# Kernel tuning notes

Hardware: AMD Instinct MI355X
Metric: run time of the kernel (lower is better)

Reference implementation:

```python
import jax, jax.numpy as jnp
import numpy as np

K = 1024
D = 256
BETA = 0.25


def setup_inputs() -> dict:
    key = jax.random.key(0)
    k1, k2 = jax.random.split(key)
    inputs = jax.random.normal(k1, (16, D, 4096), dtype=jnp.float32)  # (B, D, T)
    # embedding.weight.data.uniform_(-1/K, 1/K)
    weight = jax.random.uniform(k2, (K, D), dtype=jnp.float32, minval=-1.0 / K, maxval=1.0 / K)
    return {"inputs": inputs, "weight": weight}


def reference(inputs, weight):
    B, Dd, T = inputs.shape
    x = jnp.transpose(inputs, (0, 2, 1))          # (B, T, D)
    flat = x.reshape(-1, Dd)                      # (N, D), N = B*T
    in_sqr = jnp.sum(flat * flat, axis=1, keepdims=True)     # (N, 1)
    embed_sqr = jnp.sum(weight * weight, axis=1)             # (K,)
    dis = in_sqr + embed_sqr - 2.0 * (flat @ weight.T)       # (N, K)
    ind = jnp.argmin(dis, axis=1)                            # (N,)
    quant = weight[ind].reshape(B, T, Dd)                    # gather == one-hot @ weight
    vq = jnp.mean((jax.lax.stop_gradient(quant) - x) ** 2)
    commit = jnp.mean((quant - jax.lax.stop_gradient(x)) ** 2)
    vq_loss = BETA * vq + commit
    quant_st = x + jax.lax.stop_gradient(quant - x)          # straight-through
    N = flat.shape[0]
    counts = jnp.zeros((K,), dtype=jnp.float32).at[ind].add(1.0)
    avg_probs = counts / N
    perp = jnp.exp(-jnp.sum(avg_probs * jnp.log(avg_probs + 1e-10)))
    return jnp.transpose(quant_st, (0, 2, 1)), vq_loss, perp
```

## Files before the change

kernel.cpp:

```cpp
#include <hip/hip_runtime.h>
#include <hip/hip_bf16.h>


#define DD   256
#define KK   1024
#define TT   4096
#define BBB  16
#define NROW (BBB*TT)

typedef _Float16 half8 __attribute__((ext_vector_type(8)));
typedef float f32x4 __attribute__((ext_vector_type(4)));

__device__ __forceinline__ unsigned umaxu(unsigned a, unsigned b) { return a > b ? a : b; }
__device__ __forceinline__ unsigned uminu(unsigned a, unsigned b) { return a < b ? a : b; }

__global__ void prep(const float* __restrict__ w, _Float16* __restrict__ w16,
                     unsigned* __restrict__ counts, double* __restrict__ lsum,
                     float* __restrict__ wsq) {
    int gid = blockIdx.x * 256 + threadIdx.x;
    int k = gid >> 5;
    int c = gid & 31;
    int chunk = k >> 4, n = k & 15;
    int ks = c >> 2, q = c & 3;
    const float* src = w + (k << 8) + (c << 3);
    union { uint4 u; _Float16 h[8]; } pk;
#pragma unroll
    for (int j = 0; j < 8; ++j) pk.h[j] = (_Float16)(src[j] * 1024.0f);
    size_t dst = ((((size_t)chunk * 8 + ks) * 4 + q) * 16 + n) * 8;
    *(uint4*)(w16 + dst) = pk.u;
    if (c == 0) {
        const float4* wr4 = (const float4*)(w + (k << 8));
        float s = 0.f;
#pragma unroll 8
        for (int ii = 0; ii < 64; ++ii) {
            float4 v = wr4[ii];
            s += v.x * v.x + v.y * v.y + v.z * v.z + v.w * v.w;
        }
        wsq[k] = 512.0f * s;
    }
    if (gid < KK) counts[gid] = 0u;
    if (gid == KK) *lsum = 0.0;
}

#define XLS 257

#define XLOAD(toff) do {                                                       \
    int _dr = tid >> 3;                                                        \
    int _t4 = (tid & 7) << 2;                                                  \
    const float* _xb = x + ((size_t)b << 20) + t0 + (toff) + _t4;              \
    _Pragma("unroll")                                                          \
    for (int _pass = 0; _pass < 8; ++_pass) {                                  \
        int _d = (_pass << 5) + _dr;                                           \
        float4 _v = *(const float4*)(_xb + ((size_t)_d << 12));                \
        xt[(_t4 + 0) * XLS + _d] = _v.x;                                       \
        xt[(_t4 + 1) * XLS + _d] = _v.y;                                       \
        xt[(_t4 + 2) * XLS + _d] = _v.z;                                       \
        xt[(_t4 + 3) * XLS + _d] = _v.w;                                       \
    }                                                                          \
} while (0)

#define LOADB(PFX, chn) do {                                                   \
    const uint4* _p = wsrc + ((chn) << 9) + lane;                              \
    PFX##0 = *(const half8*)(_p);                                              \
    PFX##1 = *(const half8*)(_p + 64);                                         \
    PFX##2 = *(const half8*)(_p + 128);                                        \
    PFX##3 = *(const half8*)(_p + 192);                                        \
    PFX##4 = *(const half8*)(_p + 256);                                        \
    PFX##5 = *(const half8*)(_p + 320);                                        \
    PFX##6 = *(const half8*)(_p + 384);                                        \
    PFX##7 = *(const half8*)(_p + 448);                                        \
} while (0)

#define MFMA16(A, B, C) __builtin_amdgcn_mfma_f32_16x16x32_f16((A), (B), (C), 0, 0, 0)

#define COMPUTE(ch, PFX) do {                                                  \
    f32x4 a0 = {0.f, 0.f, 0.f, 0.f};                                           \
    f32x4 a1 = {0.f, 0.f, 0.f, 0.f};                                           \
    a0 = MFMA16(afrag[0][0], PFX##0, a0); a1 = MFMA16(afrag[1][0], PFX##0, a1);\
    a0 = MFMA16(afrag[0][1], PFX##1, a0); a1 = MFMA16(afrag[1][1], PFX##1, a1);\
    a0 = MFMA16(afrag[0][2], PFX##2, a0); a1 = MFMA16(afrag[1][2], PFX##2, a1);\
    a0 = MFMA16(afrag[0][3], PFX##3, a0); a1 = MFMA16(afrag[1][3], PFX##3, a1);\
    a0 = MFMA16(afrag[0][4], PFX##4, a0); a1 = MFMA16(afrag[1][4], PFX##4, a1);\
    a0 = MFMA16(afrag[0][5], PFX##5, a0); a1 = MFMA16(afrag[1][5], PFX##5, a1);\
    a0 = MFMA16(afrag[0][6], PFX##6, a0); a1 = MFMA16(afrag[1][6], PFX##6, a1);\
    a0 = MFMA16(afrag[0][7], PFX##7, a0); a1 = MFMA16(afrag[1][7], PFX##7, a1);\
    unsigned kg = (unsigned)(((ch) << 4) + n);                                 \
    float csub = wsql[kg];                                                     \
    _Pragma("unroll")                                                          \
    for (int i = 0; i < 4; ++i) {                                              \
        float v; unsigned p, o;                                                \
        v = fmaxf(a0[i] - csub, 0.0f);                                         \
        p = (__float_as_uint(v) & 0xFFFFFC00u) | kg;                           \
        o = b1[i];                                                             \
        b2[i] = umaxu(b2[i], uminu(p, o));                                     \
        b1[i] = umaxu(o, p);                                                   \
        v = fmaxf(a1[i] - csub, 0.0f);                                         \
        p = (__float_as_uint(v) & 0xFFFFFC00u) | kg;                           \
        o = b1[4 + i];                                                         \
        b2[4 + i] = umaxu(b2[4 + i], uminu(p, o));                             \
        b1[4 + i] = umaxu(o, p);                                               \
    }                                                                          \
} while (0)

__global__ __launch_bounds__(256, 2) void fused(const float* __restrict__ x,
                                                const float* __restrict__ w,
                                                const _Float16* __restrict__ w16,
                                                const float* __restrict__ wsq,
                                                float* __restrict__ out,
                                                unsigned* __restrict__ counts,
                                                double* __restrict__ lsum) {
    __shared__ __align__(16) float xt[32 * XLS];
    __shared__ __align__(16) float wsql[KK];
    __shared__ __align__(16) uint4 cndl[128];
    __shared__ double disl[32][4];
    __shared__ int winner[32];
    __shared__ double ldis[32];

    int tid = threadIdx.x, bid = blockIdx.x;
    int b = bid >> 5;
    int t0 = (bid & 31) << 7;
    int lane = tid & 63, wv = tid >> 6;
    int n = lane & 15, q = lane >> 4;

    ((float4*)wsql)[tid] = ((const float4*)wsq)[tid];

    half8 afrag[2][8];
#pragma unroll
    for (int p = 0; p < 4; ++p) {
        XLOAD(p << 5);
        __syncthreads();
        if (wv == p) {
#pragma unroll
            for (int mt = 0; mt < 2; ++mt) {
                int rl = (mt << 4) + n;
#pragma unroll
                for (int ks = 0; ks < 8; ++ks) {
                    const float* sp = &xt[rl * XLS + (ks << 5) + (q << 3)];
                    half8 f;
#pragma unroll
                    for (int j = 0; j < 8; ++j) f[j] = (_Float16)sp[j];
                    afrag[mt][ks] = f;
                }
            }
        }
        __syncthreads();
    }

    unsigned b1[8], b2[8];
#pragma unroll
    for (int i = 0; i < 8; ++i) { b1[i] = 0u; b2[i] = 0u; }

    const uint4* wsrc = (const uint4*)w16;
    half8 bA0, bA1, bA2, bA3, bA4, bA5, bA6, bA7;
    half8 bB0, bB1, bB2, bB3, bB4, bB5, bB6, bB7;

    LOADB(bA, 0);
    for (int ch = 0; ch < 64; ch += 2) {
        LOADB(bB, ch + 1);
        COMPUTE(ch, bA);
        if (ch + 2 < 64) LOADB(bA, ch + 2);
        COMPUTE(ch + 1, bB);
    }

#pragma unroll
    for (int s = 0; s < 8; ++s) {
        unsigned v0 = b1[s], v1 = b2[s], v2 = 0u, v3 = 0u;
#pragma unroll
        for (int m = 1; m <= 8; m <<= 1) {
            unsigned e0 = __shfl_xor(v0, m);
            unsigned e1 = __shfl_xor(v1, m);
            unsigned e2 = __shfl_xor(v2, m);
            unsigned e3 = __shfl_xor(v3, m);
#pragma unroll
            for (int u = 0; u < 4; ++u) {
                unsigned e = (u == 0) ? e0 : (u == 1) ? e1 : (u == 2) ? e2 : e3;
                unsigned t;
                t = umaxu(e, v0); e = uminu(e, v0); v0 = t;
                t = umaxu(e, v1); e = uminu(e, v1); v1 = t;
                t = umaxu(e, v2); e = uminu(e, v2); v2 = t;
                v3 = umaxu(e, v3);
            }
        }
        if (n == 0) {
            int row_local = (wv << 5) + ((s >> 2) << 4) + (q << 2) + (s & 3);
            cndl[row_local] = make_uint4(v0, v1, v2, v3);
        }
    }
    __syncthreads();

    int c = lane >> 4, dl = lane & 15;
    for (int qt = 0; qt < 4; ++qt) {
        XLOAD(qt << 5);
        __syncthreads();

#pragma unroll
        for (int rr = 0; rr < 8; ++rr) {
            int r = (wv << 3) + rr;
            unsigned ci = ((const unsigned*)cndl)[(((qt << 5) + r) << 2) + c] & 1023u;
            const float* wr = w + (ci << 8);
            double s = 0.0;
#pragma unroll
            for (int dd = 0; dd < 4; ++dd) {
                int d4 = (dd << 6) + (dl << 2);
                float4 xv = *(const float4*)(&xt[r * XLS + d4]);
                float4 wv4 = *(const float4*)(wr + d4);
                double e;
                e = (double)xv.x - (double)wv4.x; s = fma(e, e, s);
                e = (double)xv.y - (double)wv4.y; s = fma(e, e, s);
                e = (double)xv.z - (double)wv4.z; s = fma(e, e, s);
                e = (double)xv.w - (double)wv4.w; s = fma(e, e, s);
            }
#pragma unroll
            for (int m = 1; m <= 8; m <<= 1) s += __shfl_xor(s, m);
            if (dl == 0) disl[r][c] = s;
        }
        __syncthreads();

        if (tid < 32) {
            uint4 cc = cndl[(qt << 5) + tid];
            unsigned i0 = cc.x & 1023u, i1 = cc.y & 1023u, i2 = cc.z & 1023u, i3 = cc.w & 1023u;
            double dm = disl[tid][0]; unsigned ci = i0;
            double dk;
            dk = disl[tid][1]; if (dk < dm || (dk == dm && i1 < ci)) { dm = dk; ci = i1; }
            dk = disl[tid][2]; if (dk < dm || (dk == dm && i2 < ci)) { dm = dk; ci = i2; }
            dk = disl[tid][3]; if (dk < dm || (dk == dm && i3 < ci)) { dm = dk; ci = i3; }
            winner[tid] = (int)ci;
            ldis[tid] = dm;
            atomicAdd(&counts[ci], 1u);
        }
        __syncthreads();

#pragma unroll
        for (int rp = 0; rp < 8; ++rp) {
            int r = (rp << 2) + wv;
            int win = winner[r];
            *(float4*)(&xt[r * XLS + (lane << 2)]) =
                *(const float4*)(w + (win << 8) + (lane << 2));
        }
        __syncthreads();

        {
            int dr = tid >> 3;
            int t4 = (tid & 7) << 2;
            float* ob = out + ((size_t)b << 20) + t0 + (qt << 5) + t4;
#pragma unroll
            for (int pass = 0; pass < 8; ++pass) {
                int d = (pass << 5) + dr;
                float4 o;
                o.x = xt[(t4 + 0) * XLS + d];
                o.y = xt[(t4 + 1) * XLS + d];
                o.z = xt[(t4 + 2) * XLS + d];
                o.w = xt[(t4 + 3) * XLS + d];
                *(float4*)(ob + ((size_t)d << 12)) = o;
            }
        }

        __syncthreads();
        if (tid < 16) ldis[tid] += ldis[tid + 16];
        __syncthreads();
        if (tid < 8) ldis[tid] += ldis[tid + 8];
        __syncthreads();
        if (tid < 4) ldis[tid] += ldis[tid + 4];
        __syncthreads();
        if (tid < 2) ldis[tid] += ldis[tid + 2];
        __syncthreads();
        if (tid == 0) atomicAdd(lsum, ldis[0] + ldis[1]);
        __syncthreads();
    }
}

__global__ void finalize(const unsigned* __restrict__ counts,
                         const double* __restrict__ lsum,
                         float* __restrict__ out2) {
    __shared__ double part[256];
    int tid = threadIdx.x;
    double s = 0.0;
    for (int i = tid; i < KK; i += 256) {
        double p = (double)counts[i] / (double)NROW;
        s += p * log(p + 1e-10);
    }
    part[tid] = s;
    __syncthreads();
    for (int st = 128; st > 0; st >>= 1) {
        if (tid < st) part[tid] += part[tid + st];
        __syncthreads();
    }
    if (tid == 0) {
        out2[0] = (float)(1.25 * (*lsum) / ((double)NROW * (double)DD));
        out2[1] = (float)exp(-part[0]);
    }
}

extern "C" void kernel_launch(void* const* d_in, const int* in_sizes, int n_in,
                              void* d_out, int out_size, void* d_ws, size_t ws_size,
                              hipStream_t stream) {
    const float* x = (const float*)d_in[0];
    const float* w = (const float*)d_in[1];
    float* out = (float*)d_out;
    char* ws = (char*)d_ws;
    _Float16* w16    = (_Float16*)ws;
    unsigned* counts = (unsigned*)(ws + 524288);
    float*    wsq    = (float*)(ws + 528384);
    double*   lsum   = (double*)(ws + 532480);

    prep<<<128, 256, 0, stream>>>(w, w16, counts, lsum, wsq);
    fused<<<512, 256, 0, stream>>>(x, w, w16, wsq, out, counts, lsum);
    finalize<<<1, 256, 0, stream>>>(counts, lsum, out + (size_t)NROW * DD);
}
```

Measured before the change: 186.5 us.

## Double rows per block so each codebook fragment feeds four MFMA tiles

Each block now handles 256 time steps instead of 128. Each wave keeps four 16-row A tiles in registers, so every fp16 codebook fragment loaded from global memory is reused across twice as many MFMAs. This halves codebook traffic per row. The grid drops to 256 blocks, launch bounds go to 1 block per SM, and the winner-row gather is rewritten with a different lane mapping. The cost is higher register pressure (afrag doubles, 16 top-2 slots) and fewer blocks than the 256 CUs, which gives lower occupancy and less latency hiding.

```diff
diff --git a/kernel.cpp b/kernel.cpp
--- a/kernel.cpp
+++ b/kernel.cpp
@@ -73,17 +73,19 @@
 
 #define MFMA16(A, B, C) __builtin_amdgcn_mfma_f32_16x16x32_f16((A), (B), (C), 0, 0, 0)
 
-#define COMPUTE(ch, PFX) do {                                                  \
+#define MStep(KS, PFX)                                                         \
+    a0 = MFMA16(afrag[0][KS], PFX##KS, a0);                                    \
+    a1 = MFMA16(afrag[1][KS], PFX##KS, a1);                                    \
+    a2 = MFMA16(afrag[2][KS], PFX##KS, a2);                                    \
+    a3 = MFMA16(afrag[3][KS], PFX##KS, a3);
+
+#define COMPUTE4(ch, PFX) do {                                                 \
     f32x4 a0 = {0.f, 0.f, 0.f, 0.f};                                           \
     f32x4 a1 = {0.f, 0.f, 0.f, 0.f};                                           \
-    a0 = MFMA16(afrag[0][0], PFX##0, a0); a1 = MFMA16(afrag[1][0], PFX##0, a1);\
-    a0 = MFMA16(afrag[0][1], PFX##1, a0); a1 = MFMA16(afrag[1][1], PFX##1, a1);\
-    a0 = MFMA16(afrag[0][2], PFX##2, a0); a1 = MFMA16(afrag[1][2], PFX##2, a1);\
-    a0 = MFMA16(afrag[0][3], PFX##3, a0); a1 = MFMA16(afrag[1][3], PFX##3, a1);\
-    a0 = MFMA16(afrag[0][4], PFX##4, a0); a1 = MFMA16(afrag[1][4], PFX##4, a1);\
-    a0 = MFMA16(afrag[0][5], PFX##5, a0); a1 = MFMA16(afrag[1][5], PFX##5, a1);\
-    a0 = MFMA16(afrag[0][6], PFX##6, a0); a1 = MFMA16(afrag[1][6], PFX##6, a1);\
-    a0 = MFMA16(afrag[0][7], PFX##7, a0); a1 = MFMA16(afrag[1][7], PFX##7, a1);\
+    f32x4 a2 = {0.f, 0.f, 0.f, 0.f};                                           \
+    f32x4 a3 = {0.f, 0.f, 0.f, 0.f};                                           \
+    MStep(0, PFX) MStep(1, PFX) MStep(2, PFX) MStep(3, PFX)                    \
+    MStep(4, PFX) MStep(5, PFX) MStep(6, PFX) MStep(7, PFX)                    \
     unsigned kg = (unsigned)(((ch) << 4) + n);                                 \
     float csub = wsql[kg];                                                     \
     _Pragma("unroll")                                                          \
@@ -99,10 +101,20 @@
         o = b1[4 + i];                                                         \
         b2[4 + i] = umaxu(b2[4 + i], uminu(p, o));                             \
         b1[4 + i] = umaxu(o, p);                                               \
+        v = fmaxf(a2[i] - csub, 0.0f);                                         \
+        p = (__float_as_uint(v) & 0xFFFFFC00u) | kg;                           \
+        o = b1[8 + i];                                                         \
+        b2[8 + i] = umaxu(b2[8 + i], uminu(p, o));                             \
+        b1[8 + i] = umaxu(o, p);                                               \
+        v = fmaxf(a3[i] - csub, 0.0f);                                         \
+        p = (__float_as_uint(v) & 0xFFFFFC00u) | kg;                           \
+        o = b1[12 + i];                                                        \
+        b2[12 + i] = umaxu(b2[12 + i], uminu(p, o));                           \
+        b1[12 + i] = umaxu(o, p);                                              \
     }                                                                          \
 } while (0)
 
-__global__ __launch_bounds__(256, 2) void fused(const float* __restrict__ x,
+__global__ __launch_bounds__(256, 1) void fused(const float* __restrict__ x,
                                                 const float* __restrict__ w,
                                                 const _Float16* __restrict__ w16,
                                                 const float* __restrict__ wsq,
@@ -111,28 +123,30 @@
                                                 double* __restrict__ lsum) {
     __shared__ __align__(16) float xt[32 * XLS];
     __shared__ __align__(16) float wsql[KK];
-    __shared__ __align__(16) uint4 cndl[128];
+    __shared__ __align__(16) uint4 cndl[256];
     __shared__ double disl[32][4];
     __shared__ int winner[32];
     __shared__ double ldis[32];
 
     int tid = threadIdx.x, bid = blockIdx.x;
-    int b = bid >> 5;
-    int t0 = (bid & 31) << 7;
+    int b = bid >> 4;
+    int t0 = (bid & 15) << 8;
     int lane = tid & 63, wv = tid >> 6;
     int n = lane & 15, q = lane >> 4;
 
     ((float4*)wsql)[tid] = ((const float4*)wsq)[tid];
 
-    half8 afrag[2][8];
-#pragma unroll
-    for (int p = 0; p < 4; ++p) {
-        XLOAD(p << 5);
-        __syncthreads();
-        if (wv == p) {
-#pragma unroll
-            for (int mt = 0; mt < 2; ++mt) {
-                int rl = (mt << 4) + n;
+    half8 afrag[4][8];
+#pragma unroll
+    for (int q8 = 0; q8 < 8; ++q8) {
+        XLOAD(q8 << 5);
+        __syncthreads();
+        if ((q8 >> 1) == wv) {
+            const int mt_hi = q8 & 1;
+#pragma unroll
+            for (int ml = 0; ml < 2; ++ml) {
+                const int mt = (mt_hi << 1) + ml;
+                int rl = (ml << 4) + n;
 #pragma unroll
                 for (int ks = 0; ks < 8; ++ks) {
                     const float* sp = &xt[rl * XLS + (ks << 5) + (q << 3)];
@@ -146,9 +160,9 @@
         __syncthreads();
     }
 
-    unsigned b1[8], b2[8];
-#pragma unroll
-    for (int i = 0; i < 8; ++i) { b1[i] = 0u; b2[i] = 0u; }
+    unsigned b1[16], b2[16];
+#pragma unroll
+    for (int i = 0; i < 16; ++i) { b1[i] = 0u; b2[i] = 0u; }
 
     const uint4* wsrc = (const uint4*)w16;
     half8 bA0, bA1, bA2, bA3, bA4, bA5, bA6, bA7;
@@ -157,13 +171,13 @@
     LOADB(bA, 0);
     for (int ch = 0; ch < 64; ch += 2) {
         LOADB(bB, ch + 1);
-        COMPUTE(ch, bA);
+        COMPUTE4(ch, bA);
         if (ch + 2 < 64) LOADB(bA, ch + 2);
-        COMPUTE(ch + 1, bB);
-    }
-
-#pragma unroll
-    for (int s = 0; s < 8; ++s) {
+        COMPUTE4(ch + 1, bB);
+    }
+
+#pragma unroll
+    for (int s = 0; s < 16; ++s) {
         unsigned v0 = b1[s], v1 = b2[s], v2 = 0u, v3 = 0u;
 #pragma unroll
         for (int m = 1; m <= 8; m <<= 1) {
@@ -182,14 +196,15 @@
             }
         }
         if (n == 0) {
-            int row_local = (wv << 5) + ((s >> 2) << 4) + (q << 2) + (s & 3);
+            int row_local = (wv << 6) + ((s >> 2) << 4) + (q << 2) + (s & 3);
             cndl[row_local] = make_uint4(v0, v1, v2, v3);
         }
     }
     __syncthreads();
 
     int c = lane >> 4, dl = lane & 15;
-    for (int qt = 0; qt < 4; ++qt) {
+    int rr2 = lane >> 3, c8 = lane & 7;
+    for (int qt = 0; qt < 8; ++qt) {
         XLOAD(qt << 5);
         __syncthreads();
 
@@ -230,12 +245,18 @@
         }
         __syncthreads();
 
-#pragma unroll
-        for (int rp = 0; rp < 8; ++rp) {
-            int r = (rp << 2) + wv;
-            int win = winner[r];
-            *(float4*)(&xt[r * XLS + (lane << 2)]) =
-                *(const float4*)(w + (win << 8) + (lane << 2));
+        {
+            int rowr = (wv << 3) + rr2;
+            int win = winner[rowr];
+            const float* wrow = w + (win << 8);
+#pragma unroll
+            for (int cc2 = 0; cc2 < 4; ++cc2) {
+                int col = (cc2 << 6) + (c8 << 3);
+                float4 g0 = *(const float4*)(wrow + col);
+                float4 g1 = *(const float4*)(wrow + col + 4);
+                *(float4*)(&xt[rowr * XLS + col]) = g0;
+                *(float4*)(&xt[rowr * XLS + col + 4]) = g1;
+            }
         }
         __syncthreads();
 
@@ -304,6 +325,6 @@
     double*   lsum   = (double*)(ws + 532480);
 
     prep<<<128, 256, 0, stream>>>(w, w16, counts, lsum, wsq);
-    fused<<<512, 256, 0, stream>>>(x, w, w16, wsq, out, counts, lsum);
+    fused<<<256, 256, 0, stream>>>(x, w, w16, wsq, out, counts, lsum);
     finalize<<<1, 256, 0, stream>>>(counts, lsum, out + (size_t)NROW * DD);
 }
```

Result: slower. 217.8 us (+16.8%).

## Double-buffer x tiles and prefetch next tile during refinement phase

Applied to the files above, without the earlier changes.

Splits the x transpose buffer into two LDS buffers. The next 32-row x tile is prefetched into registers while the current tile is refined and written out, and the first tile's load is issued before the MFMA distance loop so its latency is hidden. It also replaces the multi-barrier shared-memory loss reduction with a single-wave shuffle reduction and uses lighter lgkm-only barriers. This doubles x LDS use (about 66KB total) and adds 32 prefetch registers, which may strain the two-blocks-per-CU occupancy target.

```diff
diff --git a/kernel.cpp b/kernel.cpp
--- a/kernel.cpp
+++ b/kernel.cpp
@@ -13,6 +13,12 @@
 
 __device__ __forceinline__ unsigned umaxu(unsigned a, unsigned b) { return a > b ? a : b; }
 __device__ __forceinline__ unsigned uminu(unsigned a, unsigned b) { return a < b ? a : b; }
+
+__device__ __forceinline__ void barrier_lgkm() {
+    asm volatile("s_waitcnt lgkmcnt(0)" ::: "memory");
+    __builtin_amdgcn_s_barrier();
+    __builtin_amdgcn_sched_barrier(0);
+}
 
 __global__ void prep(const float* __restrict__ w, _Float16* __restrict__ w16,
                      unsigned* __restrict__ counts, double* __restrict__ lsum,
@@ -44,7 +50,7 @@
 
 #define XLS 257
 
-#define XLOAD(toff) do {                                                       \
+#define XLOAD(BUF, toff) do {                                                  \
     int _dr = tid >> 3;                                                        \
     int _t4 = (tid & 7) << 2;                                                  \
     const float* _xb = x + ((size_t)b << 20) + t0 + (toff) + _t4;              \
@@ -52,11 +58,31 @@
     for (int _pass = 0; _pass < 8; ++_pass) {                                  \
         int _d = (_pass << 5) + _dr;                                           \
         float4 _v = *(const float4*)(_xb + ((size_t)_d << 12));                \
-        xt[(_t4 + 0) * XLS + _d] = _v.x;                                       \
-        xt[(_t4 + 1) * XLS + _d] = _v.y;                                       \
-        xt[(_t4 + 2) * XLS + _d] = _v.z;                                       \
-        xt[(_t4 + 3) * XLS + _d] = _v.w;                                       \
-    }                                                                          \
+        BUF[(_t4 + 0) * XLS + _d] = _v.x;                                      \
+        BUF[(_t4 + 1) * XLS + _d] = _v.y;                                      \
+        BUF[(_t4 + 2) * XLS + _d] = _v.z;                                      \
+        BUF[(_t4 + 3) * XLS + _d] = _v.w;                                      \
+    }                                                                          \
+} while (0)
+
+#define XP1(P, toff)                                                           \
+    xp##P = *(const float4*)(x + ((size_t)b << 20) + t0 + (toff) + ((tid & 7) << 2) \
+                             + ((size_t)((P << 5) + (tid >> 3)) << 12));
+#define XPREF(toff) do {                                                       \
+    XP1(0, toff) XP1(1, toff) XP1(2, toff) XP1(3, toff)                        \
+    XP1(4, toff) XP1(5, toff) XP1(6, toff) XP1(7, toff)                        \
+} while (0)
+#define XW1(P, BUF) {                                                          \
+    int _d = (P << 5) + (tid >> 3);                                            \
+    int _t4 = (tid & 7) << 2;                                                  \
+    BUF[(_t4 + 0) * XLS + _d] = xp##P.x;                                       \
+    BUF[(_t4 + 1) * XLS + _d] = xp##P.y;                                       \
+    BUF[(_t4 + 2) * XLS + _d] = xp##P.z;                                       \
+    BUF[(_t4 + 3) * XLS + _d] = xp##P.w;                                       \
+}
+#define XWRITE(BUF) do {                                                       \
+    XW1(0, BUF) XW1(1, BUF) XW1(2, BUF) XW1(3, BUF)                            \
+    XW1(4, BUF) XW1(5, BUF) XW1(6, BUF) XW1(7, BUF)                            \
 } while (0)
 
 #define LOADB(PFX, chn) do {                                                   \
@@ -102,6 +128,86 @@
     }                                                                          \
 } while (0)
 
+#define P2BODY(QT, CUR, NXT, DOPREF) do {                                      \
+    if (DOPREF) XPREF(((QT) + 1) << 5);                                        \
+    _Pragma("unroll")                                                          \
+    for (int rr = 0; rr < 8; ++rr) {                                           \
+        int r = (wv << 3) + rr;                                                \
+        unsigned ci = ((const unsigned*)cndl)[((((QT) << 5) + r) << 2) + c] & 1023u; \
+        const float* wr = w + (ci << 8);                                       \
+        double s = 0.0;                                                        \
+        _Pragma("unroll")                                                      \
+        for (int dd = 0; dd < 4; ++dd) {                                       \
+            int d4 = (dd << 6) + (dl << 2);                                    \
+            float4 xv = *(const float4*)(&CUR[r * XLS + d4]);                  \
+            float4 wv4 = *(const float4*)(wr + d4);                            \
+            double e;                                                          \
+            e = (double)xv.x - (double)wv4.x; s = fma(e, e, s);                \
+            e = (double)xv.y - (double)wv4.y; s = fma(e, e, s);                \
+            e = (double)xv.z - (double)wv4.z; s = fma(e, e, s);                \
+            e = (double)xv.w - (double)wv4.w; s = fma(e, e, s);                \
+        }                                                                      \
+        _Pragma("unroll")                                                      \
+        for (int m = 1; m <= 8; m <<= 1) s += __shfl_xor(s, m);                \
+        if (dl == 0) disl[r][cidx] = s;                                        \
+    }                                                                          \
+    barrier_lgkm();                                                            \
+    {                                                                          \
+        double dm = 0.0;                                                       \
+        if (tid < 32) {                                                        \
+            uint4 cc = cndl[((QT) << 5) + tid];                                \
+            unsigned i0 = cc.x & 1023u, i1 = cc.y & 1023u,                     \
+                     i2 = cc.z & 1023u, i3 = cc.w & 1023u;                     \
+            double dmv = disl[tid][0]; unsigned ci = i0;                       \
+            double dk;                                                         \
+            dk = disl[tid][1]; if (dk < dmv || (dk == dmv && i1 < ci)) { dmv = dk; ci = i1; } \
+            dk = disl[tid][2]; if (dk < dmv || (dk == dmv && i2 < ci)) { dmv = dk; ci = i2; } \
+            dk = disl[tid][3]; if (dk < dmv || (dk == dmv && i3 < ci)) { dmv = dk; ci = i3; } \
+            winner[tid] = (int)ci;                                             \
+            dm = dmv;                                                          \
+            atomicAdd(&counts[ci], 1u);                                        \
+        }                                                                      \
+        if (wv == 0) {                                                         \
+            dm += __shfl_xor(dm, 16); dm += __shfl_xor(dm, 8);                 \
+            dm += __shfl_xor(dm, 4);  dm += __shfl_xor(dm, 2);                 \
+            dm += __shfl_xor(dm, 1);  dm += __shfl_xor(dm, 32);                \
+            if (lane == 0) atomicAdd(lsum, dm);                                \
+        }                                                                      \
+    }                                                                          \
+    barrier_lgkm();                                                            \
+    {                                                                          \
+        int rowr = (wv << 3) + rr2;                                            \
+        int win = winner[rowr];                                                \
+        const float* wrow = w + (win << 8);                                    \
+        _Pragma("unroll")                                                      \
+        for (int cc2 = 0; cc2 < 4; ++cc2) {                                    \
+            int col = (cc2 << 6) + (c8 << 3);                                  \
+            float4 g0 = *(const float4*)(wrow + col);                          \
+            float4 g1 = *(const float4*)(wrow + col + 4);                      \
+            *(float4*)(&CUR[rowr * XLS + col]) = g0;                           \
+            *(float4*)(&CUR[rowr * XLS + col + 4]) = g1;                       \
+        }                                                                      \
+    }                                                                          \
+    barrier_lgkm();                                                            \
+    {                                                                          \
+        int dr = tid >> 3;                                                     \
+        int t4 = (tid & 7) << 2;                                               \
+        float* ob = out + ((size_t)b << 20) + t0 + ((QT) << 5) + t4;           \
+        _Pragma("unroll")                                                      \
+        for (int pass = 0; pass < 8; ++pass) {                                 \
+            int d = (pass << 5) + dr;                                          \
+            float4 o;                                                          \
+            o.x = CUR[(t4 + 0) * XLS + d];                                     \
+            o.y = CUR[(t4 + 1) * XLS + d];                                     \
+            o.z = CUR[(t4 + 2) * XLS + d];                                     \
+            o.w = CUR[(t4 + 3) * XLS + d];                                     \
+            *(float4*)(ob + ((size_t)d << 12)) = o;                            \
+        }                                                                      \
+    }                                                                          \
+    if (DOPREF) XWRITE(NXT);                                                   \
+    barrier_lgkm();                                                            \
+} while (0)
+
 __global__ __launch_bounds__(256, 2) void fused(const float* __restrict__ x,
                                                 const float* __restrict__ w,
                                                 const _Float16* __restrict__ w16,
@@ -109,12 +215,12 @@
                                                 float* __restrict__ out,
                                                 unsigned* __restrict__ counts,
                                                 double* __restrict__ lsum) {
-    __shared__ __align__(16) float xt[32 * XLS];
+    __shared__ __align__(16) float xta[32 * XLS];
+    __shared__ __align__(16) float xtb[32 * XLS];
     __shared__ __align__(16) float wsql[KK];
     __shared__ __align__(16) uint4 cndl[128];
     __shared__ double disl[32][4];
     __shared__ int winner[32];
-    __shared__ double ldis[32];
 
     int tid = threadIdx.x, bid = blockIdx.x;
     int b = bid >> 5;
@@ -127,7 +233,7 @@
     half8 afrag[2][8];
 #pragma unroll
     for (int p = 0; p < 4; ++p) {
-        XLOAD(p << 5);
+        XLOAD(xta, p << 5);
         __syncthreads();
         if (wv == p) {
 #pragma unroll
@@ -135,7 +241,7 @@
                 int rl = (mt << 4) + n;
 #pragma unroll
                 for (int ks = 0; ks < 8; ++ks) {
-                    const float* sp = &xt[rl * XLS + (ks << 5) + (q << 3)];
+                    const float* sp = &xta[rl * XLS + (ks << 5) + (q << 3)];
                     half8 f;
 #pragma unroll
                     for (int j = 0; j < 8; ++j) f[j] = (_Float16)sp[j];
@@ -145,6 +251,9 @@
         }
         __syncthreads();
     }
+
+    float4 xp0, xp1, xp2, xp3, xp4, xp5, xp6, xp7;
+    XPREF(0);
 
     unsigned b1[8], b2[8];
 #pragma unroll
@@ -186,87 +295,16 @@
             cndl[row_local] = make_uint4(v0, v1, v2, v3);
         }
     }
+    XWRITE(xta);
     __syncthreads();
 
     int c = lane >> 4, dl = lane & 15;
-    for (int qt = 0; qt < 4; ++qt) {
-        XLOAD(qt << 5);
-        __syncthreads();
-
-#pragma unroll
-        for (int rr = 0; rr < 8; ++rr) {
-            int r = (wv << 3) + rr;
-            unsigned ci = ((const unsigned*)cndl)[(((qt << 5) + r) << 2) + c] & 1023u;
-            const float* wr = w + (ci << 8);
-            double s = 0.0;
-#pragma unroll
-            for (int dd = 0; dd < 4; ++dd) {
-                int d4 = (dd << 6) + (dl << 2);
-                float4 xv = *(const float4*)(&xt[r * XLS + d4]);
-                float4 wv4 = *(const float4*)(wr + d4);
-                double e;
-                e = (double)xv.x - (double)wv4.x; s = fma(e, e, s);
-                e = (double)xv.y - (double)wv4.y; s = fma(e, e, s);
-                e = (double)xv.z - (double)wv4.z; s = fma(e, e, s);
-                e = (double)xv.w - (double)wv4.w; s = fma(e, e, s);
-            }
-#pragma unroll
-            for (int m = 1; m <= 8; m <<= 1) s += __shfl_xor(s, m);
-            if (dl == 0) disl[r][c] = s;
-        }
-        __syncthreads();
-
-        if (tid < 32) {
-            uint4 cc = cndl[(qt << 5) + tid];
-            unsigned i0 = cc.x & 1023u, i1 = cc.y & 1023u, i2 = cc.z & 1023u, i3 = cc.w & 1023u;
-            double dm = disl[tid][0]; unsigned ci = i0;
-            double dk;
-            dk = disl[tid][1]; if (dk < dm || (dk == dm && i1 < ci)) { dm = dk; ci = i1; }
-            dk = disl[tid][2]; if (dk < dm || (dk == dm && i2 < ci)) { dm = dk; ci = i2; }
-            dk = disl[tid][3]; if (dk < dm || (dk == dm && i3 < ci)) { dm = dk; ci = i3; }
-            winner[tid] = (int)ci;
-            ldis[tid] = dm;
-            atomicAdd(&counts[ci], 1u);
-        }
-        __syncthreads();
-
-#pragma unroll
-        for (int rp = 0; rp < 8; ++rp) {
-            int r = (rp << 2) + wv;
-            int win = winner[r];
-            *(float4*)(&xt[r * XLS + (lane << 2)]) =
-                *(const float4*)(w + (win << 8) + (lane << 2));
-        }
-        __syncthreads();
-
-        {
-            int dr = tid >> 3;
-            int t4 = (tid & 7) << 2;
-            float* ob = out + ((size_t)b << 20) + t0 + (qt << 5) + t4;
-#pragma unroll
-            for (int pass = 0; pass < 8; ++pass) {
-                int d = (pass << 5) + dr;
-                float4 o;
-                o.x = xt[(t4 + 0) * XLS + d];
-                o.y = xt[(t4 + 1) * XLS + d];
-                o.z = xt[(t4 + 2) * XLS + d];
-                o.w = xt[(t4 + 3) * XLS + d];
-                *(float4*)(ob + ((size_t)d << 12)) = o;
-            }
-        }
-
-        __syncthreads();
-        if (tid < 16) ldis[tid] += ldis[tid + 16];
-        __syncthreads();
-        if (tid < 8) ldis[tid] += ldis[tid + 8];
-        __syncthreads();
-        if (tid < 4) ldis[tid] += ldis[tid + 4];
-        __syncthreads();
-        if (tid < 2) ldis[tid] += ldis[tid + 2];
-        __syncthreads();
-        if (tid == 0) atomicAdd(lsum, ldis[0] + ldis[1]);
-        __syncthreads();
-    }
+    int cidx = c;
+    int rr2 = lane >> 3, c8 = lane & 7;
+    P2BODY(0, xta, xtb, 1);
+    P2BODY(1, xtb, xta, 1);
+    P2BODY(2, xta, xtb, 1);
+    P2BODY(3, xtb, xta, 0);
 }
 
 __global__ void finalize(const unsigned* __restrict__ counts,
```

Result: faster. 181.5 us (-2.7%).
